# Performance work log

Hardware: AMD Instinct MI355X
Metric: run time of the kernel (lower is better)

Reference implementation:

```python
import jax, jax.numpy as jnp
import numpy as np


def setup_inputs() -> dict:
    key = jax.random.key(0)
    ks = jax.random.split(key, 8)
    B, C, H, W = 4, 256, 56, 56
    Cq = C // 8
    s = 0.05  # small init scale for conv weights, like kaiming-ish for 1x1 convs
    return {
        "x": jax.random.normal(ks[0], (B, C, H, W), jnp.float32),
        "Wq": jax.random.normal(ks[1], (Cq, C), jnp.float32) * s,
        "bq": jax.random.normal(ks[2], (Cq,), jnp.float32) * s,
        "Wk": jax.random.normal(ks[3], (Cq, C), jnp.float32) * s,
        "bk": jax.random.normal(ks[4], (Cq,), jnp.float32) * s,
        "Wv": jax.random.normal(ks[5], (C, C), jnp.float32) * s,
        "bv": jax.random.normal(ks[6], (C,), jnp.float32) * s,
        "gamma": jax.random.normal(ks[7], (1,), jnp.float32),
    }


def reference(x, Wq, bq, Wk, bk, Wv, bv, gamma):
    B, C, H, W = x.shape
    N = H * W
    xf = x.reshape(B, C, N)  # flatten spatial

    # 1x1 convs == channel matmuls
    q = jnp.einsum('oc,bcn->bon', Wq, xf) + bq[None, :, None]   # [B,Cq,N]
    k = jnp.einsum('oc,bcn->bon', Wk, xf) + bk[None, :, None]   # [B,Cq,N]
    v = jnp.einsum('oc,bcn->bon', Wv, xf) + bv[None, :, None]   # [B,C,N]

    # lipschitz_norm from weights: u=||Q||_F, v=max row-norm of K^T, w=max row-norm of V^T
    u = jnp.linalg.norm(Wq)
    vn = jnp.max(jnp.linalg.norm(Wk.T, axis=1))
    wn = jnp.max(jnp.linalg.norm(Wv.T, axis=1))
    norm_value = jnp.maximum(u * vn, u * wn)  # maximum(u*v, v*u, u*w)

    # energy[b,i,j] = <q[:,i], k[:,j]>, scaled by custom Lipschitz norm
    energy = jnp.einsum('bci,bcj->bij', q, k) / norm_value      # [B,N,N]
    attention = jax.nn.softmax(energy, axis=-1)

    # out[b,c,i] = sum_j v[b,c,j] * attention[b,i,j]
    out = jnp.einsum('bcj,bij->bci', v, attention).reshape(B, C, H, W)

    # lipschitz_bound: exp(sqrt(3)) * sqrt(N/C) + 2*sqrt(6)
    bound = np.float32(np.exp(np.sqrt(3.0)) * np.sqrt(N / C) + 2.0 * np.sqrt(6.0))
    out = out / bound

    return gamma * out + x
```

## Files before the change

### kernel.cpp

```cpp
#include <hip/hip_runtime.h>

#define N_SP 3136
#define C_CH 256
#define CQ   32
#define NB   4
#define JT   64
#define NJT  49
#define QT   64
#define INV_BOUND 0.04051569f
#define LOG2E 1.44269504f

typedef __attribute__((ext_vector_type(8))) short bf16x8;
typedef __attribute__((ext_vector_type(4))) float f32x4;
typedef __attribute__((ext_vector_type(2))) long long l64x2;
typedef unsigned short u16;
typedef unsigned int   u32;
typedef unsigned char  u8;
typedef long long      l64;

#define MFMA16(a,b,c) __builtin_amdgcn_mfma_f32_16x16x32_bf16(a,b,c,0,0,0)
#define MFMA8(a,b,c)  __builtin_amdgcn_mfma_f32_16x16x32_bf8_fp8(a,b,c,0,0,0)

__device__ __forceinline__ u16 f2b(float f) {
    u32 u = __builtin_bit_cast(u32, f);
    u += 0x7fffu + ((u >> 16) & 1u);
    return (u16)(u >> 16);
}
__device__ __forceinline__ u8 f2fp8(float f) {
    return (u8)(__builtin_amdgcn_cvt_pk_fp8_f32(f, f, 0, false) & 0xff);
}
__device__ __forceinline__ void dma16(const void* g, void* l) {
    __builtin_amdgcn_global_load_lds((const __attribute__((address_space(1))) u32*)g,
                                     (__attribute__((address_space(3))) u32*)l, 16, 0, 0);
}

__global__ __launch_bounds__(256) void stage1_kernel(
    const float* __restrict__ x, const float* __restrict__ Wq,
    const float* __restrict__ Wk, const float* __restrict__ Wv,
    u8* __restrict__ xT, u8* __restrict__ Wqb, u8* __restrict__ Wkb,
    u8* __restrict__ Wvb, float* __restrict__ scale_out,
    float* __restrict__ kmax)
{
    __shared__ float smem[64 * 65];
    const int t = threadIdx.x;
    const int bid = blockIdx.x;

    if (bid < 784) {
        float (*tile)[65] = (float(*)[65])smem;
        const int xcd = bid & 7, slot = bid >> 3;
        const int b = xcd >> 1;
        const int i = slot * 2 + (xcd & 1);
        const int ct = i & 3, nt = i >> 2;
        const int c0 = ct * 64, n0 = nt * 64;
        const int cc = t >> 4, nn4 = (t & 15) * 4;
        #pragma unroll
        for (int k = 0; k < 4; ++k) {
            int cl = cc + k * 16;
            float4 v = *(const float4*)(x + (size_t)(b * C_CH + c0 + cl) * N_SP + n0 + nn4);
            tile[cl][nn4] = v.x; tile[cl][nn4 + 1] = v.y;
            tile[cl][nn4 + 2] = v.z; tile[cl][nn4 + 3] = v.w;
        }
        __syncthreads();
        const int c4 = (t & 15) * 4, nn = t >> 4;
        #pragma unroll
        for (int k = 0; k < 4; ++k) {
            int nl = nn + k * 16;
            ushort4 o;
            o.x = f2b(tile[c4 + 0][nl]); o.y = f2b(tile[c4 + 1][nl]);
            o.z = f2b(tile[c4 + 2][nl]); o.w = f2b(tile[c4 + 3][nl]);
            const int off = ((c0 + c4) * 2) ^ ((nl & 15) << 5);
            *(ushort4*)(xT + (size_t)(b * N_SP + n0 + nl) * 512 + off) = o;
        }
    } else if (bid < 864) {
        int idx = (bid - 784) * 256 + t;
        const float* src; u8* dst; int off;
        if (idx < 2048)      { src = Wq; dst = Wqb; off = idx; }
        else if (idx < 4096) { src = Wk; dst = Wkb; off = idx - 2048; }
        else                 { src = Wv; dst = Wvb; off = idx - 4096; }
        float4 v = *(const float4*)(src + off * 4);
        ushort4 o; o.x = f2b(v.x); o.y = f2b(v.y); o.z = f2b(v.z); o.w = f2b(v.w);
        const int row = off >> 6, inner = (off & 63) * 8;
        *(ushort4*)(dst + row * 512 + (inner ^ ((row & 15) << 5))) = o;
    } else {
        if (t < NB) kmax[t] = 0.f;
        float* red = smem;
        float u2 = 0.f;
        for (int i = t; i < CQ * C_CH; i += 256) { float w = Wq[i]; u2 += w * w; }
        red[t] = u2; __syncthreads();
        #pragma unroll
        for (int s = 128; s > 0; s >>= 1) { if (t < s) red[t] += red[t + s]; __syncthreads(); }
        float u2t = red[0]; __syncthreads();
        float vn2 = 0.f;
        for (int o = 0; o < CQ; ++o)   { float w = Wk[o * C_CH + t]; vn2 += w * w; }
        float wn2 = 0.f;
        for (int o = 0; o < C_CH; ++o) { float w = Wv[o * C_CH + t]; wn2 += w * w; }
        red[t] = fmaxf(vn2, wn2); __syncthreads();
        #pragma unroll
        for (int s = 128; s > 0; s >>= 1) { if (t < s) red[t] = fmaxf(red[t], red[t + s]); __syncthreads(); }
        if (t == 0) scale_out[0] = 1.0f / (sqrtf(u2t) * sqrtf(red[0]));
    }
}

__global__ __launch_bounds__(256) void qkv_mfma(
    const u8* __restrict__ xT, const u8* __restrict__ Wqb,
    const u8* __restrict__ Wkb, const u8* __restrict__ Wvb,
    const float* __restrict__ bq, const float* __restrict__ bk,
    const float* __restrict__ bv, const float* __restrict__ scale_p,
    u16* __restrict__ qT, u8* __restrict__ Kg, u8* __restrict__ Vg,
    float* __restrict__ qnorm, float* __restrict__ kmax)
{
    __shared__ __align__(16) u8 xTl[32768];
    __shared__ __align__(16) u8 Wl[32768];

    const int t = threadIdx.x;
    const int xcd = blockIdx.x & 7, slot = blockIdx.x >> 3;
    const int b = xcd >> 1;
    const int i = slot * 2 + (xcd & 1);
    if (i >= 245) return;
    const int split = i / 49, nt = i % 49;
    const int w = t >> 6, lane = t & 63, li = t & 15, g = (t >> 4) & 3;
    const int n = nt * 64 + w * 16 + li;
    const int r0 = (split - 1) * 64;
    const f32x4 zero = {0.f, 0.f, 0.f, 0.f};

    {
        const u8* xsrc = xT + (size_t)(b * N_SP + nt * 64) * 512;
        #pragma unroll
        for (int k = 0; k < 8; ++k)
            dma16(xsrc + w * 8192 + k * 1024 + lane * 16, xTl + w * 8192 + k * 1024);
        if (split == 0) {
            #pragma unroll
            for (int k = 0; k < 4; ++k)
                dma16(Wqb + w * 4096 + k * 1024 + lane * 16, Wl + w * 4096 + k * 1024);
            #pragma unroll
            for (int k = 0; k < 4; ++k)
                dma16(Wkb + w * 4096 + k * 1024 + lane * 16, Wl + 16384 + w * 4096 + k * 1024);
        } else {
            const u8* wsrc = Wvb + (size_t)r0 * 512;
            #pragma unroll
            for (int k = 0; k < 8; ++k)
                dma16(wsrc + w * 8192 + k * 1024 + lane * 16, Wl + w * 8192 + k * 1024);
        }
    }
    asm volatile("s_waitcnt vmcnt(0)" ::: "memory");
    __syncthreads();

    const int swz = li << 5;
    bf16x8 xf[8];
    #pragma unroll
    for (int ks = 0; ks < 8; ++ks)
        xf[ks] = *(const bf16x8*)(xTl + (w * 16 + li) * 512 + ((ks * 64 + 16 * g) ^ swz));

    if (split == 0) {
        f32x4 aq0 = zero, aq1 = zero, ak0 = zero, ak1 = zero;
        #pragma unroll
        for (int ks = 0; ks < 8; ++ks) {
            const int o = (ks * 64 + 16 * g) ^ swz;
            bf16x8 w0 = *(const bf16x8*)(Wl + li * 512 + o);
            bf16x8 w1 = *(const bf16x8*)(Wl + (16 + li) * 512 + o);
            bf16x8 w2 = *(const bf16x8*)(Wl + 16384 + li * 512 + o);
            bf16x8 w3 = *(const bf16x8*)(Wl + 16384 + (16 + li) * 512 + o);
            aq0 = MFMA16(w0, xf[ks], aq0);
            aq1 = MFMA16(w1, xf[ks], aq1);
            ak0 = MFMA16(w2, xf[ks], ak0);
            ak1 = MFMA16(w3, xf[ks], ak1);
        }
        const float scf = scale_p[0] * LOG2E;
        f32x4 bq0 = *(const f32x4*)(bq + 4 * g);
        f32x4 bq1 = *(const f32x4*)(bq + 16 + 4 * g);
        f32x4 bk0 = *(const f32x4*)(bk + 4 * g);
        f32x4 bk1 = *(const f32x4*)(bk + 16 + 4 * g);
        float qn2 = 0.f, kn2 = 0.f;
        ushort4 s0, s1;
        #pragma unroll
        for (int r = 0; r < 4; ++r) {
            float q0 = (aq0[r] + bq0[r]) * scf;
            float q1 = (aq1[r] + bq1[r]) * scf;
            qn2 += q0 * q0 + q1 * q1;
            ((u16*)&s0)[r] = f2b(q0); ((u16*)&s1)[r] = f2b(q1);
        }
        *(ushort4*)(qT + (size_t)(b * N_SP + n) * CQ + 4 * g)      = s0;
        *(ushort4*)(qT + (size_t)(b * N_SP + n) * CQ + 16 + 4 * g) = s1;
        #pragma unroll
        for (int r = 0; r < 4; ++r) {
            float k0 = ak0[r] + bk0[r];
            float k1 = ak1[r] + bk1[r];
            kn2 += k0 * k0 + k1 * k1;
            ((u16*)&s0)[r] = f2b(k0); ((u16*)&s1)[r] = f2b(k1);
        }
        u8* krow = Kg + ((size_t)b * N_SP + n) * 64;
        const int swn = ((n >> 1) & 3) << 4;
        *(ushort4*)(krow + ((8 * g) ^ swn))      = s0;
        *(ushort4*)(krow + ((32 + 8 * g) ^ swn)) = s1;

        qn2 += __shfl_xor(qn2, 16); qn2 += __shfl_xor(qn2, 32);
        kn2 += __shfl_xor(kn2, 16); kn2 += __shfl_xor(kn2, 32);
        if (g == 0) qnorm[b * N_SP + n] = sqrtf(qn2);
        float kn = sqrtf(kn2);
        #pragma unroll
        for (int d = 1; d < 16; d <<= 1) kn = fmaxf(kn, __shfl_xor(kn, d));
        if ((t & 63) == 0) atomicMax((int*)(kmax + b), __float_as_int(kn));
    } else {
        f32x4 a[4] = {zero, zero, zero, zero};
        #pragma unroll
        for (int ks = 0; ks < 8; ++ks) {
            const int o = (ks * 64 + 16 * g) ^ swz;
            #pragma unroll
            for (int fr = 0; fr < 4; ++fr) {
                bf16x8 wf = *(const bf16x8*)(Wl + (fr * 16 + li) * 512 + o);
                a[fr] = MFMA16(wf, xf[ks], a[fr]);
            }
        }
        const int jj = w * 16 + li;
        const int p = ((jj >> 5) & 1) * 8 + ((jj >> 3) & 3) * 16 + (jj & 7);
        u8* vtile = Vg + (size_t)(b * NJT + nt) * 16384;
        #pragma unroll
        for (int fr = 0; fr < 4; ++fr) {
            f32x4 bb = *(const f32x4*)(bv + r0 + fr * 16 + 4 * g);
            #pragma unroll
            for (int r = 0; r < 4; ++r) {
                const int c = r0 + fr * 16 + 4 * g + r;
                vtile[c * 64 + (p ^ (((c >> 1) & 3) << 4))] = f2fp8(a[fr][r] + bb[r]);
            }
        }
    }
}

__global__ __launch_bounds__(1024) void attn_mfma(
    const u16* __restrict__ qT, const u8* __restrict__ Kg,
    const u8* __restrict__ Vg, const float* __restrict__ x,
    const float* __restrict__ gamma_p, const float* __restrict__ qnorm,
    const float* __restrict__ kmax, float* __restrict__ out)
{
    __shared__ __align__(16) u8 smem[86016];
    u8* const Vl = smem;
    u8* const Kl = smem + 65536;
    u8* const Pl = smem + 81920;

    const int t = threadIdx.x;
    const int w = t >> 6, li = t & 15, g = (t >> 4) & 3;
    const int jh = w & 3, qh = w >> 2;
    const int swz = ((li >> 1) & 3) << 4;

    const int b  = blockIdx.x / NJT;
    const int qt = blockIdx.x % NJT;
    const int i0 = qt * QT;

    const u16* qTb = qT + (size_t)b * N_SP * CQ;
    const u8*  Kbb = Kg + (size_t)b * N_SP * 64;
    const u8*  Vbb = Vg + (size_t)b * NJT * 16384;
    const float kmb = kmax[b];
    const f32x4 zero = {0.f, 0.f, 0.f, 0.f};

    const bf16x8 qf = *(const bf16x8*)(qTb + (size_t)(i0 + qh * 16 + li) * CQ + 8 * g);
    const float  mr = qnorm[b * N_SP + i0 + qh * 16 + li] * kmb;

    f32x4 acc[4];
    #pragma unroll
    for (int qq = 0; qq < 4; ++qq) acc[qq] = zero;
    float ls = 0.f;

    #define ISSUE(jt_, s_) do {                                               \
        dma16(Vbb + (size_t)(jt_) * 16384 + t * 16,                           \
              Vl + (s_) * 16384 + w * 1024);                                  \
        if (t < 256)                                                          \
            dma16(Kbb + (size_t)(jt_) * 4096 + t * 16,                        \
                  Kl + (s_) * 4096 + w * 1024);                               \
    } while (0)

    ISSUE(0, 0);
    ISSUE(1, 1);
    ISSUE(2, 2);

    const int p0 = ((jh >> 1) & 1) * 8 + ((jh * 2 + (g >> 1)) & 3) * 16 + 4 * (g & 1);

    for (int it = 0; it < NJT; ++it) {
        const int cur = it & 3;
        if (w < 4) asm volatile("s_waitcnt vmcnt(4) lgkmcnt(0)" ::: "memory");
        else       asm volatile("s_waitcnt vmcnt(2) lgkmcnt(0)" ::: "memory");
        __builtin_amdgcn_s_barrier();
        asm volatile("" ::: "memory");

        {
            int jn = it + 3; if (jn > NJT - 1) jn = NJT - 1;
            ISSUE(jn, (cur + 3) & 3);
        }

        const u8* Kc = Kl + cur * 4096;
        bf16x8 kf = *(const bf16x8*)(Kc + (jh * 16 + li) * 64 + ((16 * g) ^ swz));
        f32x4 s = MFMA16(kf, qf, zero);
        {
            float a0 = exp2f(s[0] - mr), a1 = exp2f(s[1] - mr);
            float a2 = exp2f(s[2] - mr), a3 = exp2f(s[3] - mr);
            ls += (a0 + a1) + (a2 + a3);
            int pk = __builtin_amdgcn_cvt_pk_bf8_f32(a0, a1, 0, false);
            pk = __builtin_amdgcn_cvt_pk_bf8_f32(a2, a3, pk, true);
            *(u32*)(Pl + (qh * 16 + li) * 64 + (p0 ^ swz)) = (u32)pk;
        }
        asm volatile("s_waitcnt lgkmcnt(0)" ::: "memory");
        __builtin_amdgcn_s_barrier();
        asm volatile("" ::: "memory");

        const u8* Vc = Vl + cur * 16384;
        __builtin_amdgcn_s_setprio(1);
        l64x2 pa0 = *(const l64x2*)(Pl + (0 * 16 + li) * 64 + ((16 * g) ^ swz));
        l64x2 pa1 = *(const l64x2*)(Pl + (1 * 16 + li) * 64 + ((16 * g) ^ swz));
        l64x2 pa2 = *(const l64x2*)(Pl + (2 * 16 + li) * 64 + ((16 * g) ^ swz));
        l64x2 pa3 = *(const l64x2*)(Pl + (3 * 16 + li) * 64 + ((16 * g) ^ swz));
        l64x2 v0  = *(const l64x2*)(Vc + (w * 16 + li) * 64 + ((16 * g) ^ swz));
        acc[0] = MFMA8(pa0[0], v0[0], acc[0]);
        acc[1] = MFMA8(pa1[0], v0[0], acc[1]);
        acc[2] = MFMA8(pa2[0], v0[0], acc[2]);
        acc[3] = MFMA8(pa3[0], v0[0], acc[3]);
        acc[0] = MFMA8(pa0[1], v0[1], acc[0]);
        acc[1] = MFMA8(pa1[1], v0[1], acc[1]);
        acc[2] = MFMA8(pa2[1], v0[1], acc[2]);
        acc[3] = MFMA8(pa3[1], v0[1], acc[3]);
        __builtin_amdgcn_s_setprio(0);
    }
    #undef ISSUE

    ls += __shfl_xor(ls, 16); ls += __shfl_xor(ls, 32);
    __syncthreads();
    float* red       = (float*)Pl;
    float* red_final = (float*)(Pl + 1024);
    if ((t & 63) < 16) red[w * 16 + li] = ls;
    __syncthreads();
    if (t < 64) {
        const int qh2 = t >> 4, l2 = t & 15;
        float s = red[(qh2 * 4 + 0) * 16 + l2] + red[(qh2 * 4 + 1) * 16 + l2]
                + red[(qh2 * 4 + 2) * 16 + l2] + red[(qh2 * 4 + 3) * 16 + l2];
        red_final[t] = s;
    }
    __syncthreads();

    const float gsc = gamma_p[0] * INV_BOUND;
    const int c = w * 16 + li;
    #pragma unroll
    for (int qq = 0; qq < 4; ++qq) {
        f32x4 lsv = *(const f32x4*)(red_final + qq * 16 + 4 * g);
        f32x4 rinv;
        #pragma unroll
        for (int r = 0; r < 4; ++r) rinv[r] = gsc / lsv[r];
        const size_t base = ((size_t)b * C_CH + c) * N_SP + i0 + qq * 16 + 4 * g;
        float4 xv = *(const float4*)(x + base);
        float4 o;
        o.x = acc[qq][0] * rinv[0] + xv.x;
        o.y = acc[qq][1] * rinv[1] + xv.y;
        o.z = acc[qq][2] * rinv[2] + xv.z;
        o.w = acc[qq][3] * rinv[3] + xv.w;
        *(float4*)(out + base) = o;
    }
}

extern "C" void kernel_launch(void* const* d_in, const int* in_sizes, int n_in,
                              void* d_out, int out_size, void* d_ws, size_t ws_size,
                              hipStream_t stream)
{
    const float* x  = (const float*)d_in[0];
    const float* Wq = (const float*)d_in[1];
    const float* bq = (const float*)d_in[2];
    const float* Wk = (const float*)d_in[3];
    const float* bk = (const float*)d_in[4];
    const float* Wv = (const float*)d_in[5];
    const float* bv = (const float*)d_in[6];
    const float* gm = (const float*)d_in[7];
    float* out = (float*)d_out;
    float* ws  = (float*)d_ws;

    float* scale = ws;
    float* kmax  = ws + 4;
    float* qnorm = ws + 8;
    u8* Wqb = (u8*)(ws + 8 + NB * N_SP);
    u8* Wkb = Wqb + 32 * 512;
    u8* Wvb = Wkb + 32 * 512;
    u8* xT  = Wvb + 256 * 512;
    u16* qT = (u16*)(xT + (size_t)NB * N_SP * 512);
    u8* Kg  = (u8*)(qT + (size_t)NB * N_SP * CQ);
    u8* Vg  = Kg + (size_t)NB * N_SP * 64;

    stage1_kernel<<<865, 256, 0, stream>>>(x, Wq, Wk, Wv, xT, Wqb, Wkb, Wvb, scale, kmax);
    qkv_mfma<<<984, 256, 0, stream>>>(xT, Wqb, Wkb, Wvb, bq, bk, bv, scale, qT, Kg, Vg, qnorm, kmax);
    attn_mfma<<<196, 1024, 0, stream>>>(qT, Kg, Vg, x, gm, qnorm, kmax, out);
}
```

Measured before the change: 85.57 us.

## Software-pipeline attention loop with double-buffered P tile, one barrier per step

Restructures the main loop so the PV MFMA phase of tile it-1 and the QK/softmax phase of tile it run between the same pair of barriers. The P tile is double-buffered in LDS, which removes the second barrier per iteration. Prefetch depth drops from three tiles ahead to two so that the four-stage K/V ring stays safe. Shared memory grows slightly, and the shallower prefetch may expose more global load latency.

```diff
diff --git a/kernel.cpp b/kernel.cpp
--- a/kernel.cpp
+++ b/kernel.cpp
@@ -232,7 +232,7 @@
     const float* __restrict__ gamma_p, const float* __restrict__ qnorm,
     const float* __restrict__ kmax, float* __restrict__ out)
 {
-    __shared__ __align__(16) u8 smem[86016];
+    __shared__ __align__(16) u8 smem[90112];
     u8* const Vl = smem;
     u8* const Kl = smem + 65536;
     u8* const Pl = smem + 81920;
@@ -268,57 +268,70 @@
                   Kl + (s_) * 4096 + w * 1024);                               \
     } while (0)
 
+    #define SPHASE(it_) do {                                                  \
+        const u8* Kc_ = Kl + ((it_) & 3) * 4096;                              \
+        bf16x8 kf_ = *(const bf16x8*)(Kc_ + (jh * 16 + li) * 64 + ((16 * g) ^ swz)); \
+        f32x4 s_ = MFMA16(kf_, qf, zero);                                     \
+        float a0_ = exp2f(s_[0] - mr), a1_ = exp2f(s_[1] - mr);               \
+        float a2_ = exp2f(s_[2] - mr), a3_ = exp2f(s_[3] - mr);               \
+        ls += (a0_ + a1_) + (a2_ + a3_);                                      \
+        int pk_ = __builtin_amdgcn_cvt_pk_bf8_f32(a0_, a1_, 0, false);        \
+        pk_ = __builtin_amdgcn_cvt_pk_bf8_f32(a2_, a3_, pk_, true);           \
+        *(u32*)(Pl + ((it_) & 1) * 4096 + (qh * 16 + li) * 64 + (p0 ^ swz)) = (u32)pk_; \
+    } while (0)
+
+    #define PVPHASE(it_) do {                                                 \
+        const u8* Pp_ = Pl + ((it_) & 1) * 4096;                              \
+        const u8* Vc_ = Vl + ((it_) & 3) * 16384;                             \
+        __builtin_amdgcn_s_setprio(1);                                        \
+        l64x2 pa0_ = *(const l64x2*)(Pp_ + (0 * 16 + li) * 64 + ((16 * g) ^ swz)); \
+        l64x2 pa1_ = *(const l64x2*)(Pp_ + (1 * 16 + li) * 64 + ((16 * g) ^ swz)); \
+        l64x2 pa2_ = *(const l64x2*)(Pp_ + (2 * 16 + li) * 64 + ((16 * g) ^ swz)); \
+        l64x2 pa3_ = *(const l64x2*)(Pp_ + (3 * 16 + li) * 64 + ((16 * g) ^ swz)); \
+        l64x2 v0_  = *(const l64x2*)(Vc_ + (w * 16 + li) * 64 + ((16 * g) ^ swz)); \
+        acc[0] = MFMA8(pa0_[0], v0_[0], acc[0]);                              \
+        acc[1] = MFMA8(pa1_[0], v0_[0], acc[1]);                              \
+        acc[2] = MFMA8(pa2_[0], v0_[0], acc[2]);                              \
+        acc[3] = MFMA8(pa3_[0], v0_[0], acc[3]);                              \
+        acc[0] = MFMA8(pa0_[1], v0_[1], acc[0]);                              \
+        acc[1] = MFMA8(pa1_[1], v0_[1], acc[1]);                              \
+        acc[2] = MFMA8(pa2_[1], v0_[1], acc[2]);                              \
+        acc[3] = MFMA8(pa3_[1], v0_[1], acc[3]);                              \
+        __builtin_amdgcn_s_setprio(0);                                        \
+    } while (0)
+
     ISSUE(0, 0);
     ISSUE(1, 1);
+
+    const int p0 = ((jh >> 1) & 1) * 8 + ((jh * 2 + (g >> 1)) & 3) * 16 + 4 * (g & 1);
+
+    if (w < 4) asm volatile("s_waitcnt vmcnt(2) lgkmcnt(0)" ::: "memory");
+    else       asm volatile("s_waitcnt vmcnt(1) lgkmcnt(0)" ::: "memory");
+    __builtin_amdgcn_s_barrier();
+    asm volatile("" ::: "memory");
     ISSUE(2, 2);
-
-    const int p0 = ((jh >> 1) & 1) * 8 + ((jh * 2 + (g >> 1)) & 3) * 16 + 4 * (g & 1);
-
-    for (int it = 0; it < NJT; ++it) {
-        const int cur = it & 3;
-        if (w < 4) asm volatile("s_waitcnt vmcnt(4) lgkmcnt(0)" ::: "memory");
-        else       asm volatile("s_waitcnt vmcnt(2) lgkmcnt(0)" ::: "memory");
+    SPHASE(0);
+
+    for (int it = 1; it < NJT; ++it) {
+        if (w < 4) asm volatile("s_waitcnt vmcnt(2) lgkmcnt(0)" ::: "memory");
+        else       asm volatile("s_waitcnt vmcnt(1) lgkmcnt(0)" ::: "memory");
         __builtin_amdgcn_s_barrier();
         asm volatile("" ::: "memory");
-
         {
-            int jn = it + 3; if (jn > NJT - 1) jn = NJT - 1;
-            ISSUE(jn, (cur + 3) & 3);
-        }
-
-        const u8* Kc = Kl + cur * 4096;
-        bf16x8 kf = *(const bf16x8*)(Kc + (jh * 16 + li) * 64 + ((16 * g) ^ swz));
-        f32x4 s = MFMA16(kf, qf, zero);
-        {
-            float a0 = exp2f(s[0] - mr), a1 = exp2f(s[1] - mr);
-            float a2 = exp2f(s[2] - mr), a3 = exp2f(s[3] - mr);
-            ls += (a0 + a1) + (a2 + a3);
-            int pk = __builtin_amdgcn_cvt_pk_bf8_f32(a0, a1, 0, false);
-            pk = __builtin_amdgcn_cvt_pk_bf8_f32(a2, a3, pk, true);
-            *(u32*)(Pl + (qh * 16 + li) * 64 + (p0 ^ swz)) = (u32)pk;
-        }
-        asm volatile("s_waitcnt lgkmcnt(0)" ::: "memory");
-        __builtin_amdgcn_s_barrier();
-        asm volatile("" ::: "memory");
-
-        const u8* Vc = Vl + cur * 16384;
-        __builtin_amdgcn_s_setprio(1);
-        l64x2 pa0 = *(const l64x2*)(Pl + (0 * 16 + li) * 64 + ((16 * g) ^ swz));
-        l64x2 pa1 = *(const l64x2*)(Pl + (1 * 16 + li) * 64 + ((16 * g) ^ swz));
-        l64x2 pa2 = *(const l64x2*)(Pl + (2 * 16 + li) * 64 + ((16 * g) ^ swz));
-        l64x2 pa3 = *(const l64x2*)(Pl + (3 * 16 + li) * 64 + ((16 * g) ^ swz));
-        l64x2 v0  = *(const l64x2*)(Vc + (w * 16 + li) * 64 + ((16 * g) ^ swz));
-        acc[0] = MFMA8(pa0[0], v0[0], acc[0]);
-        acc[1] = MFMA8(pa1[0], v0[0], acc[1]);
-        acc[2] = MFMA8(pa2[0], v0[0], acc[2]);
-        acc[3] = MFMA8(pa3[0], v0[0], acc[3]);
-        acc[0] = MFMA8(pa0[1], v0[1], acc[0]);
-        acc[1] = MFMA8(pa1[1], v0[1], acc[1]);
-        acc[2] = MFMA8(pa2[1], v0[1], acc[2]);
-        acc[3] = MFMA8(pa3[1], v0[1], acc[3]);
-        __builtin_amdgcn_s_setprio(0);
-    }
+            int jn = it + 2; if (jn > NJT - 1) jn = NJT - 1;
+            ISSUE(jn, (it + 2) & 3);
+        }
+        PVPHASE(it - 1);
+        SPHASE(it);
+    }
+
+    asm volatile("s_waitcnt lgkmcnt(0)" ::: "memory");
+    __builtin_amdgcn_s_barrier();
+    asm volatile("" ::: "memory");
+    PVPHASE(NJT - 1);
     #undef ISSUE
+    #undef SPHASE
+    #undef PVPHASE
 
     ls += __shfl_xor(ls, 16); ls += __shfl_xor(ls, 32);
     __syncthreads();
```

Measured after the change: 82.31 us. 3.8% less time.
